# Kernel tuning notes

Measured on AMD Instinct MI355X. Metric: run time of the kernel, lower is better.

The kernel has to match this reference:

```python
import jax, jax.numpy as jnp
import numpy as np

N = 50000
E = 400000
NFEAT = 256
NHID = 64
HEADS = [4, 4, 4]
NCLASS = 121
NEG_SLOPE = 0.2


def gat_conv(h, W, al, ar, src, dst, H, D):
    # h: [N, F_in], W: [F_in, H*D], al/ar: [H, D]
    feat = (h @ W).reshape(N, H, D)                    # [N, H, D]
    el = jnp.sum(feat * al[None], axis=-1)             # [N, H]
    er = jnp.sum(feat * ar[None], axis=-1)             # [N, H]
    e = jax.nn.leaky_relu(el[src] + er[dst], NEG_SLOPE)  # [E, H]
    # edge softmax over incoming edges of each dst node
    m = jax.ops.segment_max(e, dst, num_segments=N)    # [N, H]
    ex = jnp.exp(e - m[dst])                           # [E, H]
    s = jax.ops.segment_sum(ex, dst, num_segments=N)   # [N, H]
    alpha = ex / s[dst]                                # [E, H]
    msg = alpha[..., None] * feat[src]                 # [E, H, D]
    return jax.ops.segment_sum(msg, dst, num_segments=N)  # [N, H, D]


def setup_inputs() -> dict:
    key = jax.random.key(0)
    ks = jax.random.split(key, 12)
    d = {
        "h": jax.random.normal(ks[0], (N, NFEAT), dtype=jnp.float32),
        "src": jax.random.randint(ks[1], (E,), 0, N),
        "dst": jax.random.randint(ks[2], (E,), 0, N),
        "W1": jax.random.normal(ks[3], (NFEAT, HEADS[0] * NHID), dtype=jnp.float32) * 0.05,
        "al1": jax.random.normal(ks[4], (HEADS[0], NHID), dtype=jnp.float32) * 0.1,
        "ar1": jax.random.normal(ks[5], (HEADS[0], NHID), dtype=jnp.float32) * 0.1,
        "W2": jax.random.normal(ks[6], (HEADS[0] * NHID, HEADS[1] * NHID), dtype=jnp.float32) * 0.05,
        "al2": jax.random.normal(ks[7], (HEADS[1], NHID), dtype=jnp.float32) * 0.1,
        "ar2": jax.random.normal(ks[8], (HEADS[1], NHID), dtype=jnp.float32) * 0.1,
        "W3": jax.random.normal(ks[9], (HEADS[1] * NHID, HEADS[2] * NCLASS), dtype=jnp.float32) * 0.05,
        "al3": jax.random.normal(ks[10], (HEADS[2], NCLASS), dtype=jnp.float32) * 0.1,
        "ar3": jax.random.normal(ks[11], (HEADS[2], NCLASS), dtype=jnp.float32) * 0.1,
    }
    return d


def reference(h, src, dst, W1, al1, ar1, W2, al2, ar2, W3, al3, ar3):
    # layer 1: [N, H0, NHID] -> flatten -> ELU (norm='none', drop=0, residual='none')
    x = gat_conv(h, W1, al1, ar1, src, dst, HEADS[0], NHID).reshape(N, -1)
    x = jax.nn.elu(x)
    # layer 2
    x = gat_conv(x, W2, al2, ar2, src, dst, HEADS[1], NHID).reshape(N, -1)
    x = jax.nn.elu(x)
    # output layer: mean over heads
    x = gat_conv(x, W3, al3, ar3, src, dst, HEADS[2], NCLASS).mean(axis=1)
    return x
```

## Files before the change

kernel.cpp:

```cpp
#include <hip/hip_runtime.h>
#include <cstddef>

#define NN 50000
#define NE 400000
#define NH 4
#define NC 121
#define MAXSLOT 600000

typedef __attribute__((ext_vector_type(8))) short short8;
typedef __attribute__((ext_vector_type(4))) float f32x4;
typedef __attribute__((ext_vector_type(2))) float f32x2;

static __device__ __forceinline__ unsigned short f2bf(float f) {
    unsigned u = __float_as_uint(f);
    u += 0x7fffu + ((u >> 16) & 1u);
    return (unsigned short)(u >> 16);
}
static __device__ __forceinline__ float bf2f(unsigned short u) {
    return __uint_as_float(((unsigned)u) << 16);
}
static __device__ __forceinline__ f32x2 bfpair(unsigned u) {
    f32x2 r;
    r.x = __uint_as_float(u << 16);
    r.y = __uint_as_float(u & 0xffff0000u);
    return r;
}

__global__ __launch_bounds__(256) void cast_x(const float* __restrict__ in,
                                              unsigned short* __restrict__ out, int n4) {
    int i = blockIdx.x * blockDim.x + threadIdx.x;
    if (i >= n4) return;
    float4 v = *(const float4*)&in[i * 4];
    ushort4 o;
    o.x = f2bf(v.x); o.y = f2bf(v.y); o.z = f2bf(v.z); o.w = f2bf(v.w);
    *(ushort4*)&out[i * 4] = o;
}

__global__ __launch_bounds__(256) void cast_BT(const float* __restrict__ B,
                                               unsigned short* __restrict__ BT,
                                               int N, int Npad) {
    int i = blockIdx.x * blockDim.x + threadIdx.x;
    if (i >= Npad * 256) return;
    int n = i >> 8, k = i & 255;
    float v = (n < N) ? B[(size_t)k * N + n] : 0.f;
    BT[i] = f2bf(v);
}

__global__ __launch_bounds__(256) void cast_BTcat(const float* __restrict__ W3,
                                                  unsigned short* __restrict__ BT) {
    int i = blockIdx.x * blockDim.x + threadIdx.x;
    if (i >= 128 * 1024) return;
    int c = i >> 10, kk = i & 1023;
    int h = kk >> 8, k = kk & 255;
    float v = (c < NC) ? 0.25f * W3[(size_t)k * 484 + h * NC + c] : 0.f;
    BT[i] = f2bf(v);
}

__global__ __launch_bounds__(256) void wvec3_k(const float* __restrict__ W3,
                                               const float* __restrict__ al3,
                                               const float* __restrict__ ar3,
                                               float* __restrict__ wl3,
                                               float* __restrict__ wr3) {
    int i = blockIdx.x * blockDim.x + threadIdx.x;
    if (i >= 2048) return;
    int j = i & 1023;
    int h = j >> 8, k = j & 255;
    const float* a = (i < 1024) ? al3 : ar3;
    const float* wrow = W3 + (size_t)k * 484 + h * NC;
    const float* arow = a + h * NC;
    float s = 0.f;
    for (int d = 0; d < NC; ++d) s += wrow[d] * arow[d];
    if (i < 1024) wl3[j] = s; else wr3[j] = s;
}

__global__ __launch_bounds__(256) void gemm_bf16(const unsigned short* __restrict__ A,
                                                 const unsigned short* __restrict__ BT,
                                                 float* __restrict__ Cf,
                                                 unsigned short* __restrict__ Cb,
                                                 const float* __restrict__ al,
                                                 const float* __restrict__ ar,
                                                 float* __restrict__ el,
                                                 float* __restrict__ er,
                                                 int M, int Nout, int K) {
    __shared__ __align__(16) unsigned short Alds[128 * 32];
    __shared__ __align__(16) unsigned short Blds[128 * 32];
    const int tid = threadIdx.x;
    const int wave = tid >> 6;
    const int lane = tid & 63;
    const int quad = lane >> 4;
    const int ml = lane & 15;
    const int m0 = blockIdx.x * 128;
    const int n0 = blockIdx.y * 128;
    const int wm0 = (wave >> 1) * 64;
    const int wn0 = (wave & 1) * 64;
    const int r = tid >> 2;
    const int c8 = (tid & 3) * 8;

    f32x4 acc[4][4] = {};

    for (int k0 = 0; k0 < K; k0 += 32) {
        #pragma unroll
        for (int p = 0; p < 2; ++p) {
            int rr = r + p * 64;
            int m = m0 + rr;
            uint4 va = make_uint4(0u, 0u, 0u, 0u);
            if (m < M) va = *(const uint4*)&A[(size_t)m * K + k0 + c8];
            *(uint4*)&Alds[rr * 32 + c8] = va;
            int n = n0 + rr;
            uint4 vb = *(const uint4*)&BT[(size_t)n * K + k0 + c8];
            *(uint4*)&Blds[rr * 32 + c8] = vb;
        }
        __syncthreads();

        short8 af[4], bf[4];
        #pragma unroll
        for (int i = 0; i < 4; ++i)
            af[i] = *(const short8*)&Alds[(wm0 + i * 16 + ml) * 32 + quad * 8];
        #pragma unroll
        for (int j = 0; j < 4; ++j)
            bf[j] = *(const short8*)&Blds[(wn0 + j * 16 + ml) * 32 + quad * 8];
        #pragma unroll
        for (int i = 0; i < 4; ++i)
            #pragma unroll
            for (int j = 0; j < 4; ++j)
                acc[i][j] = __builtin_amdgcn_mfma_f32_16x16x32_bf16(af[i], bf[j], acc[i][j], 0, 0, 0);
        __syncthreads();
    }

    #pragma unroll
    for (int i = 0; i < 4; ++i) {
        #pragma unroll
        for (int reg = 0; reg < 4; ++reg) {
            int m = m0 + wm0 + i * 16 + quad * 4 + reg;
            if (m >= M) continue;
            #pragma unroll
            for (int j = 0; j < 4; ++j) {
                int n = n0 + wn0 + j * 16 + ml;
                if (n < Nout) {
                    if (Cb) Cb[(size_t)m * Nout + n] = f2bf(acc[i][j][reg]);
                    else    Cf[(size_t)m * Nout + n] = acc[i][j][reg];
                }
            }
        }
    }

    if (el) {
        int head = (n0 + wn0) >> 6;
        float alv[4], arv[4];
        #pragma unroll
        for (int j = 0; j < 4; ++j) {
            alv[j] = al[head * 64 + j * 16 + ml];
            arv[j] = ar[head * 64 + j * 16 + ml];
        }
        #pragma unroll
        for (int i = 0; i < 4; ++i) {
            #pragma unroll
            for (int reg = 0; reg < 4; ++reg) {
                float sl = 0.f, sr = 0.f;
                #pragma unroll
                for (int j = 0; j < 4; ++j) {
                    float v = acc[i][j][reg];
                    sl += v * alv[j];
                    sr += v * arv[j];
                }
                #pragma unroll
                for (int off = 1; off < 16; off <<= 1) {
                    sl += __shfl_xor(sl, off);
                    sr += __shfl_xor(sr, off);
                }
                int m = m0 + wm0 + i * 16 + quad * 4 + reg;
                if (ml == 0 && m < M) {
                    el[m * 4 + head] = sl;
                    er[m * 4 + head] = sr;
                }
            }
        }
    }
}

__global__ __launch_bounds__(256) void hist_k(const int* __restrict__ dst, int* __restrict__ deg) {
    int e = blockIdx.x * blockDim.x + threadIdx.x;
    if (e < NE) atomicAdd(&deg[dst[e]], 1);
}

__global__ __launch_bounds__(256) void scan1(const int* __restrict__ deg,
                                             int* __restrict__ excl,
                                             int* __restrict__ partials) {
    __shared__ int sh[256];
    int i = blockIdx.x * 256 + threadIdx.x;
    int v = (i < NN) ? ((deg[i] + 3) & ~3) : 0;
    sh[threadIdx.x] = v;
    __syncthreads();
    for (int off = 1; off < 256; off <<= 1) {
        int t = (threadIdx.x >= off) ? sh[threadIdx.x - off] : 0;
        __syncthreads();
        sh[threadIdx.x] += t;
        __syncthreads();
    }
    if (i < NN) excl[i] = sh[threadIdx.x] - v;
    if (threadIdx.x == 255) partials[blockIdx.x] = sh[255];
}

__global__ __launch_bounds__(256) void scan2(int* __restrict__ partials, int nb) {
    __shared__ int sh[256];
    int t = threadIdx.x;
    int v = (t < nb) ? partials[t] : 0;
    sh[t] = v;
    __syncthreads();
    for (int off = 1; off < 256; off <<= 1) {
        int x = (t >= off) ? sh[t - off] : 0;
        __syncthreads();
        sh[t] += x;
        __syncthreads();
    }
    if (t < nb) partials[t] = sh[t] - v;
}

__global__ __launch_bounds__(256) void scan3(const int* __restrict__ excl,
                                             const int* __restrict__ partials,
                                             int* __restrict__ rowptr) {
    int i = blockIdx.x * 256 + threadIdx.x;
    if (i < NN) rowptr[i] = excl[i] + partials[blockIdx.x];
}

__global__ __launch_bounds__(256) void scatter_k(const int* __restrict__ src,
                                                 const int* __restrict__ dst,
                                                 const int* __restrict__ rowptr,
                                                 int* __restrict__ cursor,
                                                 int* __restrict__ ssrc,
                                                 int* __restrict__ sdst) {
    int e = blockIdx.x * blockDim.x + threadIdx.x;
    if (e >= NE) return;
    int d = dst[e];
    int p = atomicAdd(&cursor[d], 1);
    int pos = rowptr[d] + p;
    ssrc[pos] = src[e];
    sdst[pos] = d;
}

__global__ __launch_bounds__(256) void edgew_k(const int* __restrict__ ssrc,
                                               const int* __restrict__ sdst,
                                               const float* __restrict__ el,
                                               const float* __restrict__ er,
                                               float* __restrict__ wcsr) {
    int i = blockIdx.x * blockDim.x + threadIdx.x;
    if (i >= MAXSLOT) return;
    int d = sdst[i];
    float w0 = 0.f, w1 = 0.f, w2 = 0.f, w3 = 0.f;
    if (d >= 0) {
        int s = ssrc[i];
        float4 e_l = *(const float4*)&el[s * 4];
        float4 e_r = *(const float4*)&er[d * 4];
        float v0 = e_l.x + e_r.x; v0 = fmaxf(v0, 0.2f * v0);
        float v1 = e_l.y + e_r.y; v1 = fmaxf(v1, 0.2f * v1);
        float v2 = e_l.z + e_r.z; v2 = fmaxf(v2, 0.2f * v2);
        float v3 = e_l.w + e_r.w; v3 = fmaxf(v3, 0.2f * v3);
        w0 = __expf(v0); w1 = __expf(v1); w2 = __expf(v2); w3 = __expf(v3);
    }
    wcsr[0 * MAXSLOT + i] = w0;
    wcsr[1 * MAXSLOT + i] = w1;
    wcsr[2 * MAXSLOT + i] = w2;
    wcsr[3 * MAXSLOT + i] = w3;
}

__global__ __launch_bounds__(256) void agg256(const int* __restrict__ rowptr,
                                              const int* __restrict__ deg,
                                              const int* __restrict__ ssrc,
                                              const float* __restrict__ wcsr,
                                              const unsigned short* __restrict__ feat,
                                              unsigned short* __restrict__ ybf,
                                              const float* __restrict__ wl3,
                                              const float* __restrict__ wr3,
                                              float* __restrict__ el3,
                                              float* __restrict__ er3) {
    int wid = (blockIdx.x * blockDim.x + threadIdx.x) >> 6;
    int lane = threadIdx.x & 63;
    if (wid >= NN) return;
    int n = wid;
    int start = rowptr[n];
    int cnt4 = (deg[n] + 3) & ~3;
    int head = lane >> 4;
    const float* wch = wcsr + (size_t)head * MAXSLOT;
    f32x2 a01 = {0.f, 0.f}, a23 = {0.f, 0.f};
    float ssum = 0.f;
    for (int k = 0; k < cnt4; k += 4) {
        int4 sv = *(const int4*)&ssrc[start + k];
        float4 w4 = *(const float4*)&wch[start + k];
        uint2 u0 = *(const uint2*)&feat[(size_t)sv.x * 256 + lane * 4];
        uint2 u1 = *(const uint2*)&feat[(size_t)sv.y * 256 + lane * 4];
        uint2 u2 = *(const uint2*)&feat[(size_t)sv.z * 256 + lane * 4];
        uint2 u3 = *(const uint2*)&feat[(size_t)sv.w * 256 + lane * 4];
        ssum += (w4.x + w4.y) + (w4.z + w4.w);
        a01 += w4.x * bfpair(u0.x); a23 += w4.x * bfpair(u0.y);
        a01 += w4.y * bfpair(u1.x); a23 += w4.y * bfpair(u1.y);
        a01 += w4.z * bfpair(u2.x); a23 += w4.z * bfpair(u2.y);
        a01 += w4.w * bfpair(u3.x); a23 += w4.w * bfpair(u3.y);
    }
    float inv = ssum > 0.f ? 1.0f / ssum : 0.f;
    float r0 = a01.x * inv, r1 = a01.y * inv, r2 = a23.x * inv, r3 = a23.y * inv;
    r0 = r0 > 0.f ? r0 : (__expf(r0) - 1.f);
    r1 = r1 > 0.f ? r1 : (__expf(r1) - 1.f);
    r2 = r2 > 0.f ? r2 : (__expf(r2) - 1.f);
    r3 = r3 > 0.f ? r3 : (__expf(r3) - 1.f);
    ushort4 o;
    o.x = f2bf(r0); o.y = f2bf(r1); o.z = f2bf(r2); o.w = f2bf(r3);
    *(ushort4*)&ybf[(size_t)n * 256 + lane * 4] = o;

    if (wl3) {
        float sl[4], sr[4];
        #pragma unroll
        for (int h = 0; h < 4; ++h) {
            float4 a4 = *(const float4*)&wl3[h * 256 + lane * 4];
            float4 b4 = *(const float4*)&wr3[h * 256 + lane * 4];
            sl[h] = r0 * a4.x + r1 * a4.y + r2 * a4.z + r3 * a4.w;
            sr[h] = r0 * b4.x + r1 * b4.y + r2 * b4.z + r3 * b4.w;
        }
        #pragma unroll
        for (int off = 32; off; off >>= 1) {
            #pragma unroll
            for (int h = 0; h < 4; ++h) {
                sl[h] += __shfl_xor(sl[h], off);
                sr[h] += __shfl_xor(sr[h], off);
            }
        }
        if (lane == 0) {
            #pragma unroll
            for (int h = 0; h < 4; ++h) {
                el3[n * 4 + h] = sl[h];
                er3[n * 4 + h] = sr[h];
            }
        }
    }
}

__global__ __launch_bounds__(256) void agg3(const int* __restrict__ rowptr,
                                            const int* __restrict__ deg,
                                            const int* __restrict__ ssrc,
                                            const float* __restrict__ wcsr,
                                            const unsigned short* __restrict__ x,
                                            unsigned short* __restrict__ xagg) {
    int wid = (blockIdx.x * blockDim.x + threadIdx.x) >> 6;
    int lane = threadIdx.x & 63;
    if (wid >= NN) return;
    int n = wid;
    int start = rowptr[n];
    int cnt4 = (deg[n] + 3) & ~3;
    f32x2 accA[4] = {}, accB[4] = {};
    float ssum[4] = {};
    for (int k = 0; k < cnt4; k += 4) {
        int4 sv = *(const int4*)&ssrc[start + k];
        float4 w0 = *(const float4*)&wcsr[0 * MAXSLOT + start + k];
        float4 w1 = *(const float4*)&wcsr[1 * MAXSLOT + start + k];
        float4 w2 = *(const float4*)&wcsr[2 * MAXSLOT + start + k];
        float4 w3 = *(const float4*)&wcsr[3 * MAXSLOT + start + k];
        uint2 u0 = *(const uint2*)&x[(size_t)sv.x * 256 + lane * 4];
        uint2 u1 = *(const uint2*)&x[(size_t)sv.y * 256 + lane * 4];
        uint2 u2 = *(const uint2*)&x[(size_t)sv.z * 256 + lane * 4];
        uint2 u3 = *(const uint2*)&x[(size_t)sv.w * 256 + lane * 4];
        ssum[0] += (w0.x + w0.y) + (w0.z + w0.w);
        ssum[1] += (w1.x + w1.y) + (w1.z + w1.w);
        ssum[2] += (w2.x + w2.y) + (w2.z + w2.w);
        ssum[3] += (w3.x + w3.y) + (w3.z + w3.w);
        f32x2 fa = bfpair(u0.x), fA = bfpair(u0.y);
        f32x2 fb = bfpair(u1.x), fB = bfpair(u1.y);
        f32x2 fc = bfpair(u2.x), fC = bfpair(u2.y);
        f32x2 fd = bfpair(u3.x), fD = bfpair(u3.y);
        accA[0] += w0.x * fa + w0.y * fb + w0.z * fc + w0.w * fd;
        accB[0] += w0.x * fA + w0.y * fB + w0.z * fC + w0.w * fD;
        accA[1] += w1.x * fa + w1.y * fb + w1.z * fc + w1.w * fd;
        accB[1] += w1.x * fA + w1.y * fB + w1.z * fC + w1.w * fD;
        accA[2] += w2.x * fa + w2.y * fb + w2.z * fc + w2.w * fd;
        accB[2] += w2.x * fA + w2.y * fB + w2.z * fC + w2.w * fD;
        accA[3] += w3.x * fa + w3.y * fb + w3.z * fc + w3.w * fd;
        accB[3] += w3.x * fA + w3.y * fB + w3.z * fC + w3.w * fD;
    }
    #pragma unroll
    for (int h = 0; h < 4; ++h) {
        float inv = ssum[h] > 0.f ? 1.f / ssum[h] : 0.f;
        ushort4 o;
        o.x = f2bf(accA[h].x * inv); o.y = f2bf(accA[h].y * inv);
        o.z = f2bf(accB[h].x * inv); o.w = f2bf(accB[h].y * inv);
        *(ushort4*)&xagg[(size_t)n * 1024 + h * 256 + lane * 4] = o;
    }
}

extern "C" void kernel_launch(void* const* d_in, const int* in_sizes, int n_in,
                              void* d_out, int out_size, void* d_ws, size_t ws_size,
                              hipStream_t stream) {
    const float* h   = (const float*)d_in[0];
    const int*   src = (const int*)d_in[1];
    const int*   dst = (const int*)d_in[2];
    const float* W1  = (const float*)d_in[3];
    const float* al1 = (const float*)d_in[4];
    const float* ar1 = (const float*)d_in[5];
    const float* W2  = (const float*)d_in[6];
    const float* al2 = (const float*)d_in[7];
    const float* ar2 = (const float*)d_in[8];
    const float* W3  = (const float*)d_in[9];
    const float* al3 = (const float*)d_in[10];
    const float* ar3 = (const float*)d_in[11];
    float* out = (float*)d_out;

    float* ws = (float*)d_ws;
    unsigned short* x_bf    = (unsigned short*)ws;
    unsigned short* h_bf    = (unsigned short*)(ws + 6400000);
    unsigned short* feat_bf = (unsigned short*)(ws + 12800000);
    unsigned short* xagg    = (unsigned short*)(ws + 6400000);
    float* el  = ws + 32000000;
    float* er  = ws + 32200000;
    float* wl3 = ws + 32400000;
    float* wr3 = ws + 32401024;
    unsigned short* BT1   = (unsigned short*)(ws + 32402048);
    unsigned short* BT2   = (unsigned short*)(ws + 32434816);
    unsigned short* BTcat = (unsigned short*)(ws + 32467584);
    float* wcsr = ws + 32533120;
    int* ibase  = (int*)(ws + 34933120);
    int* deg      = ibase;
    int* cursor   = ibase + 50000;
    int* excl     = ibase + 100000;
    int* partials = ibase + 150000;
    int* rowptr   = ibase + 150256;
    int* ssrc     = ibase + 200256;
    int* sdst     = ibase + 800256;

    const int NB = (NN + 255) / 256;
    const int SLOT_BLOCKS = (MAXSLOT + 255) / 256;

    hipMemsetAsync(deg, 0, 2 * NN * sizeof(int), stream);
    hipMemsetAsync(ssrc, 0, MAXSLOT * sizeof(int), stream);
    hipMemsetAsync(sdst, 0xFF, MAXSLOT * sizeof(int), stream);
    hist_k<<<(NE + 255) / 256, 256, 0, stream>>>(dst, deg);
    scan1<<<NB, 256, 0, stream>>>(deg, excl, partials);
    scan2<<<1, 256, 0, stream>>>(partials, NB);
    scan3<<<NB, 256, 0, stream>>>(excl, partials, rowptr);
    scatter_k<<<(NE + 255) / 256, 256, 0, stream>>>(src, dst, rowptr, cursor, ssrc, sdst);

    cast_x<<<(NN * 256 / 4 + 255) / 256, 256, 0, stream>>>(h, h_bf, NN * 256 / 4);
    cast_BT<<<(256 * 256 + 255) / 256, 256, 0, stream>>>(W1, BT1, 256, 256);
    cast_BT<<<(256 * 256 + 255) / 256, 256, 0, stream>>>(W2, BT2, 256, 256);
    cast_BTcat<<<512, 256, 0, stream>>>(W3, BTcat);
    wvec3_k<<<8, 256, 0, stream>>>(W3, al3, ar3, wl3, wr3);

    dim3 g256((NN + 127) / 128, 2);
    dim3 gOut((NN + 127) / 128, 1);
    const int WAVE_BLOCKS = (NN * 64 + 255) / 256;

    gemm_bf16<<<g256, 256, 0, stream>>>(h_bf, BT1, nullptr, feat_bf, al1, ar1, el, er, NN, 256, 256);
    edgew_k<<<SLOT_BLOCKS, 256, 0, stream>>>(ssrc, sdst, el, er, wcsr);
    agg256<<<WAVE_BLOCKS, 256, 0, stream>>>(rowptr, deg, ssrc, wcsr, feat_bf, x_bf,
                                            nullptr, nullptr, nullptr, nullptr);

    gemm_bf16<<<g256, 256, 0, stream>>>(x_bf, BT2, nullptr, feat_bf, al2, ar2, el, er, NN, 256, 256);
    edgew_k<<<SLOT_BLOCKS, 256, 0, stream>>>(ssrc, sdst, el, er, wcsr);
    agg256<<<WAVE_BLOCKS, 256, 0, stream>>>(rowptr, deg, ssrc, wcsr, feat_bf, x_bf,
                                            wl3, wr3, el, er);

    edgew_k<<<SLOT_BLOCKS, 256, 0, stream>>>(ssrc, sdst, el, er, wcsr);
    agg3<<<WAVE_BLOCKS, 256, 0, stream>>>(rowptr, deg, ssrc, wcsr, x_bf, xagg);
    gemm_bf16<<<gOut, 256, 0, stream>>>(xagg, BTcat, out, nullptr, nullptr, nullptr, nullptr, nullptr, NN, NC, 1024);
}
```

Baseline: 434.0 us.

## Merge prep casts into one kernel, use direct global-to-LDS loads, prescale source indices

The five small preprocessing kernels are merged into one launch, which cuts launch overhead. The GEMM tile loads now use global_load_lds to copy global memory straight into LDS without passing through registers. This drops the M bounds check, so the last partial tile may read past the end of A. Source indices are stored pre-shifted into byte offsets, which removes index multiplies in the edge-weight and aggregation gathers.

```diff
diff --git a/kernel.cpp b/kernel.cpp
--- a/kernel.cpp
+++ b/kernel.cpp
@@ -25,52 +25,60 @@
     r.y = __uint_as_float(u & 0xffff0000u);
     return r;
 }
-
-__global__ __launch_bounds__(256) void cast_x(const float* __restrict__ in,
-                                              unsigned short* __restrict__ out, int n4) {
+static __device__ __forceinline__ void load_lds16(const unsigned short* g, unsigned short* l) {
+    __builtin_amdgcn_global_load_lds(
+        (const __attribute__((address_space(1))) unsigned*)g,
+        (__attribute__((address_space(3))) unsigned*)l, 16, 0, 0);
+}
+
+#define PREP_X    3200000
+#define PREP_BT1  (PREP_X + 65536)
+#define PREP_BT2  (PREP_BT1 + 65536)
+#define PREP_CAT  (PREP_BT2 + 131072)
+#define PREP_WV   (PREP_CAT + 2048)
+__global__ __launch_bounds__(256) void prep_k(const float* __restrict__ h,
+                                              const float* __restrict__ W1,
+                                              const float* __restrict__ W2,
+                                              const float* __restrict__ W3,
+                                              const float* __restrict__ al3,
+                                              const float* __restrict__ ar3,
+                                              unsigned short* __restrict__ h_bf,
+                                              unsigned short* __restrict__ BT1,
+                                              unsigned short* __restrict__ BT2,
+                                              unsigned short* __restrict__ BTcat,
+                                              float* __restrict__ wl3,
+                                              float* __restrict__ wr3) {
     int i = blockIdx.x * blockDim.x + threadIdx.x;
-    if (i >= n4) return;
-    float4 v = *(const float4*)&in[i * 4];
-    ushort4 o;
-    o.x = f2bf(v.x); o.y = f2bf(v.y); o.z = f2bf(v.z); o.w = f2bf(v.w);
-    *(ushort4*)&out[i * 4] = o;
-}
-
-__global__ __launch_bounds__(256) void cast_BT(const float* __restrict__ B,
-                                               unsigned short* __restrict__ BT,
-                                               int N, int Npad) {
-    int i = blockIdx.x * blockDim.x + threadIdx.x;
-    if (i >= Npad * 256) return;
-    int n = i >> 8, k = i & 255;
-    float v = (n < N) ? B[(size_t)k * N + n] : 0.f;
-    BT[i] = f2bf(v);
-}
-
-__global__ __launch_bounds__(256) void cast_BTcat(const float* __restrict__ W3,
-                                                  unsigned short* __restrict__ BT) {
-    int i = blockIdx.x * blockDim.x + threadIdx.x;
-    if (i >= 128 * 1024) return;
-    int c = i >> 10, kk = i & 1023;
-    int h = kk >> 8, k = kk & 255;
-    float v = (c < NC) ? 0.25f * W3[(size_t)k * 484 + h * NC + c] : 0.f;
-    BT[i] = f2bf(v);
-}
-
-__global__ __launch_bounds__(256) void wvec3_k(const float* __restrict__ W3,
-                                               const float* __restrict__ al3,
-                                               const float* __restrict__ ar3,
-                                               float* __restrict__ wl3,
-                                               float* __restrict__ wr3) {
-    int i = blockIdx.x * blockDim.x + threadIdx.x;
-    if (i >= 2048) return;
-    int j = i & 1023;
-    int h = j >> 8, k = j & 255;
-    const float* a = (i < 1024) ? al3 : ar3;
-    const float* wrow = W3 + (size_t)k * 484 + h * NC;
-    const float* arow = a + h * NC;
-    float s = 0.f;
-    for (int d = 0; d < NC; ++d) s += wrow[d] * arow[d];
-    if (i < 1024) wl3[j] = s; else wr3[j] = s;
+    if (i < PREP_X) {
+        float4 v = *(const float4*)&h[(size_t)i * 4];
+        ushort4 o;
+        o.x = f2bf(v.x); o.y = f2bf(v.y); o.z = f2bf(v.z); o.w = f2bf(v.w);
+        *(ushort4*)&h_bf[(size_t)i * 4] = o;
+    } else if (i < PREP_BT1) {
+        int j = i - PREP_X;
+        int n = j >> 8, k = j & 255;
+        BT1[j] = f2bf(W1[(size_t)k * 256 + n]);
+    } else if (i < PREP_BT2) {
+        int j = i - PREP_BT1;
+        int n = j >> 8, k = j & 255;
+        BT2[j] = f2bf(W2[(size_t)k * 256 + n]);
+    } else if (i < PREP_CAT) {
+        int j = i - PREP_BT2;
+        int c = j >> 10, kk = j & 1023;
+        int hh = kk >> 8, k = kk & 255;
+        float v = (c < NC) ? 0.25f * W3[(size_t)k * 484 + hh * NC + c] : 0.f;
+        BTcat[j] = f2bf(v);
+    } else if (i < PREP_WV) {
+        int j = (i - PREP_CAT) & 1023;
+        int sel = (i - PREP_CAT) >> 10;
+        int hh = j >> 8, k = j & 255;
+        const float* a = sel ? ar3 : al3;
+        const float* wrow = W3 + (size_t)k * 484 + hh * NC;
+        const float* arow = a + hh * NC;
+        float s = 0.f;
+        for (int d = 0; d < NC; ++d) s += wrow[d] * arow[d];
+        if (sel) wr3[j] = s; else wl3[j] = s;
+    }
 }
 
 __global__ __launch_bounds__(256) void gemm_bf16(const unsigned short* __restrict__ A,
@@ -93,22 +101,19 @@
     const int n0 = blockIdx.y * 128;
     const int wm0 = (wave >> 1) * 64;
     const int wn0 = (wave & 1) * 64;
-    const int r = tid >> 2;
-    const int c8 = (tid & 3) * 8;
+
+    const unsigned short* Ab = A + (size_t)(m0 + wave * 16 + (lane >> 2)) * K + (lane & 3) * 8;
+    const unsigned short* Bb = BT + (size_t)(n0 + wave * 16 + (lane >> 2)) * K + (lane & 3) * 8;
+    unsigned short* AldsW = Alds + wave * 512;
+    unsigned short* BldsW = Blds + wave * 512;
 
     f32x4 acc[4][4] = {};
 
     for (int k0 = 0; k0 < K; k0 += 32) {
         #pragma unroll
         for (int p = 0; p < 2; ++p) {
-            int rr = r + p * 64;
-            int m = m0 + rr;
-            uint4 va = make_uint4(0u, 0u, 0u, 0u);
-            if (m < M) va = *(const uint4*)&A[(size_t)m * K + k0 + c8];
-            *(uint4*)&Alds[rr * 32 + c8] = va;
-            int n = n0 + rr;
-            uint4 vb = *(const uint4*)&BT[(size_t)n * K + k0 + c8];
-            *(uint4*)&Blds[rr * 32 + c8] = vb;
+            load_lds16(Ab + (size_t)(p * 64) * K + k0, AldsW + p * 2048);
+            load_lds16(Bb + (size_t)(p * 64) * K + k0, BldsW + p * 2048);
         }
         __syncthreads();
 
@@ -234,7 +239,7 @@
     int d = dst[e];
     int p = atomicAdd(&cursor[d], 1);
     int pos = rowptr[d] + p;
-    ssrc[pos] = src[e];
+    ssrc[pos] = src[e] << 9;
     sdst[pos] = d;
 }
 
@@ -248,8 +253,8 @@
     int d = sdst[i];
     float w0 = 0.f, w1 = 0.f, w2 = 0.f, w3 = 0.f;
     if (d >= 0) {
-        int s = ssrc[i];
-        float4 e_l = *(const float4*)&el[s * 4];
+        int su = ssrc[i];
+        float4 e_l = *(const float4*)((const char*)el + (su >> 5));
         float4 e_r = *(const float4*)&er[d * 4];
         float v0 = e_l.x + e_r.x; v0 = fmaxf(v0, 0.2f * v0);
         float v1 = e_l.y + e_r.y; v1 = fmaxf(v1, 0.2f * v1);
@@ -281,15 +286,16 @@
     int cnt4 = (deg[n] + 3) & ~3;
     int head = lane >> 4;
     const float* wch = wcsr + (size_t)head * MAXSLOT;
+    const char* fbase = (const char*)feat + lane * 8;
     f32x2 a01 = {0.f, 0.f}, a23 = {0.f, 0.f};
     float ssum = 0.f;
     for (int k = 0; k < cnt4; k += 4) {
         int4 sv = *(const int4*)&ssrc[start + k];
         float4 w4 = *(const float4*)&wch[start + k];
-        uint2 u0 = *(const uint2*)&feat[(size_t)sv.x * 256 + lane * 4];
-        uint2 u1 = *(const uint2*)&feat[(size_t)sv.y * 256 + lane * 4];
-        uint2 u2 = *(const uint2*)&feat[(size_t)sv.z * 256 + lane * 4];
-        uint2 u3 = *(const uint2*)&feat[(size_t)sv.w * 256 + lane * 4];
+        uint2 u0 = *(const uint2*)(fbase + sv.x);
+        uint2 u1 = *(const uint2*)(fbase + sv.y);
+        uint2 u2 = *(const uint2*)(fbase + sv.z);
+        uint2 u3 = *(const uint2*)(fbase + sv.w);
         ssum += (w4.x + w4.y) + (w4.z + w4.w);
         a01 += w4.x * bfpair(u0.x); a23 += w4.x * bfpair(u0.y);
         a01 += w4.y * bfpair(u1.x); a23 += w4.y * bfpair(u1.y);
@@ -345,6 +351,7 @@
     int n = wid;
     int start = rowptr[n];
     int cnt4 = (deg[n] + 3) & ~3;
+    const char* xbase = (const char*)x + lane * 8;
     f32x2 accA[4] = {}, accB[4] = {};
     float ssum[4] = {};
     for (int k = 0; k < cnt4; k += 4) {
@@ -353,10 +360,10 @@
         float4 w1 = *(const float4*)&wcsr[1 * MAXSLOT + start + k];
         float4 w2 = *(const float4*)&wcsr[2 * MAXSLOT + start + k];
         float4 w3 = *(const float4*)&wcsr[3 * MAXSLOT + start + k];
-        uint2 u0 = *(const uint2*)&x[(size_t)sv.x * 256 + lane * 4];
-        uint2 u1 = *(const uint2*)&x[(size_t)sv.y * 256 + lane * 4];
-        uint2 u2 = *(const uint2*)&x[(size_t)sv.z * 256 + lane * 4];
-        uint2 u3 = *(const uint2*)&x[(size_t)sv.w * 256 + lane * 4];
+        uint2 u0 = *(const uint2*)(xbase + sv.x);
+        uint2 u1 = *(const uint2*)(xbase + sv.y);
+        uint2 u2 = *(const uint2*)(xbase + sv.z);
+        uint2 u3 = *(const uint2*)(xbase + sv.w);
         ssum[0] += (w0.x + w0.y) + (w0.z + w0.w);
         ssum[1] += (w1.x + w1.y) + (w1.z + w1.w);
         ssum[2] += (w2.x + w2.y) + (w2.z + w2.w);
@@ -435,11 +442,8 @@
     scan3<<<NB, 256, 0, stream>>>(excl, partials, rowptr);
     scatter_k<<<(NE + 255) / 256, 256, 0, stream>>>(src, dst, rowptr, cursor, ssrc, sdst);
 
-    cast_x<<<(NN * 256 / 4 + 255) / 256, 256, 0, stream>>>(h, h_bf, NN * 256 / 4);
-    cast_BT<<<(256 * 256 + 255) / 256, 256, 0, stream>>>(W1, BT1, 256, 256);
-    cast_BT<<<(256 * 256 + 255) / 256, 256, 0, stream>>>(W2, BT2, 256, 256);
-    cast_BTcat<<<512, 256, 0, stream>>>(W3, BTcat);
-    wvec3_k<<<8, 256, 0, stream>>>(W3, al3, ar3, wl3, wr3);
+    prep_k<<<(PREP_WV + 255) / 256, 256, 0, stream>>>(h, W1, W2, W3, al3, ar3,
+                                                      h_bf, BT1, BT2, BTcat, wl3, wr3);
 
     dim3 g256((NN + 127) / 128, 2);
     dim3 gOut((NN + 127) / 128, 1);
```

New measurement: 413.3 us. 4.8% less time.
